# Optimization experiments

Measured on AMD Instinct MI355X. Metric: run time of the kernel, lower is better.

The kernel has to match this reference:

```python
import jax, jax.numpy as jnp
import numpy as np

B, T, C = 8, 2048, 1024
E = 8            # num_experts (= world_size in the original)
K = 2            # top-k
CAP_FACTOR = 1.25
CAPACITY = int(T / E * CAP_FACTOR)  # 320, per (expert, batch-row)
DFF = 4 * C


def setup_inputs() -> dict:
    key = jax.random.key(0)
    ks = jax.random.split(key, 4)
    x = jax.random.normal(ks[0], (B, T, C), dtype=jnp.float32)
    Wg = jax.random.normal(ks[1], (C, E), dtype=jnp.float32) * (C ** -0.5)
    bg = jnp.zeros((E,), dtype=jnp.float32)
    W1 = jax.random.normal(ks[2], (E, C, DFF), dtype=jnp.float32) * (C ** -0.5)
    b1 = jnp.zeros((E, DFF), dtype=jnp.float32)
    W2 = jax.random.normal(ks[3], (E, DFF, C), dtype=jnp.float32) * (DFF ** -0.5)
    b2 = jnp.zeros((E, C), dtype=jnp.float32)
    return {"x": x, "Wg": Wg, "bg": bg, "W1": W1, "b1": b1, "W2": W2, "b2": b2}


def reference(x, Wg, bg, W1, b1, W2, b2):
    # Router: linear + softmax, then top-k gating
    probs = jax.nn.softmax(jnp.einsum('btc,ce->bte', x, Wg) + bg, axis=-1)  # [B,T,E]
    topk_p, topk_e = jax.lax.top_k(probs, K)                               # [B,T,K]

    S = T * K  # one "assignment" per (token, k-slot), row-major (t, k) order
    e_flat = topk_e.reshape(B, S)                      # expert id per assignment
    p_flat = topk_p.reshape(B, S)

    # Position of each assignment within its (batch-row, expert) group,
    # ordered by token position then k-slot (matches nonzero() row-major order).
    onehot = (e_flat[..., None] == jnp.arange(E)).astype(jnp.int32)        # [B,S,E]
    pos_all = jnp.cumsum(onehot, axis=1) - 1                                # [B,S,E]
    pos = jnp.take_along_axis(pos_all, e_flat[..., None], axis=2)[..., 0]   # [B,S]
    keep = pos < CAPACITY                               # overflow tokens are dropped

    # Dispatch tokens into padded per-(expert,row) buffers: [E,B,CAPACITY,C]
    x_rep = jnp.repeat(x, K, axis=1)                    # [B,S,C], assignment order
    b_idx = jnp.broadcast_to(jnp.arange(B)[:, None], (B, S))
    pos_scat = jnp.where(keep, pos, CAPACITY)           # out-of-range -> dropped
    dispatch = jnp.zeros((E, B, CAPACITY, C), dtype=x.dtype)
    dispatch = dispatch.at[e_flat, b_idx, pos_scat].set(x_rep, mode='drop')

    # Grouped expert FFN (padding rows are zeros; their outputs are never read back)
    h = jax.nn.relu(jnp.einsum('ebsc,ech->ebsh', dispatch, W1) + b1[:, None, None, :])
    y = jnp.einsum('ebsh,ehc->ebsc', h, W2) + b2[:, None, None, :]

    # Combine: gather back, scale by gate prob (dropped tokens -> padding_val 0)
    gathered = y[e_flat, b_idx, jnp.clip(pos, 0, CAPACITY - 1)]             # [B,S,C]
    out = gathered * jnp.where(keep, p_flat, 0.0)[..., None]
    return out.reshape(B, T, K, C).sum(axis=2)          # sum over k assignments
```

## Files before the change

### kernel.cpp

```cpp
#include <hip/hip_runtime.h>
#include <stdint.h>

#define B_ 8
#define T_ 2048
#define C_ 1024
#define E_ 8
#define K_ 2
#define CAP_ 320
#define DFF_ 4096
#define S_ (T_*K_)
#define NTOK (B_*T_)
#define ROWS_PER_E (B_*CAP_)

typedef __attribute__((ext_vector_type(8))) short short8;
typedef __attribute__((ext_vector_type(4))) float floatx4;

__device__ __forceinline__ unsigned short f2bf(float f) {
  union { float f; unsigned u; } v; v.f = f;
  unsigned r = v.u + 0x7fffu + ((v.u >> 16) & 1u);
  return (unsigned short)(r >> 16);
}
__device__ __forceinline__ float bf2f(unsigned short h) {
  union { unsigned u; float f; } v; v.u = ((unsigned)h) << 16;
  return v.f;
}

#define GLOAD16(g, l) __builtin_amdgcn_global_load_lds( \
    (const __attribute__((address_space(1))) void*)(g), \
    (__attribute__((address_space(3))) void*)(l), 16, 0, 0)

__global__ void router_kernel(const float* __restrict__ x, const float* __restrict__ Wg,
                              const float* __restrict__ bg,
                              int* __restrict__ topk_e, float* __restrict__ topk_p)
{
  int token = (int)((blockIdx.x * blockDim.x + threadIdx.x) >> 6);
  int lane = threadIdx.x & 63;
  if (token >= NTOK) return;
  const float* xr = x + (size_t)token * C_;
  double acc[E_];
  #pragma unroll
  for (int e = 0; e < E_; ++e) acc[e] = 0.0;
  for (int c = lane; c < C_; c += 64) {
    double xv = (double)xr[c];
    const float4* w4 = (const float4*)(Wg + (size_t)c * E_);
    float4 wa = w4[0], wb = w4[1];
    acc[0] += xv * (double)wa.x; acc[1] += xv * (double)wa.y;
    acc[2] += xv * (double)wa.z; acc[3] += xv * (double)wa.w;
    acc[4] += xv * (double)wb.x; acc[5] += xv * (double)wb.y;
    acc[6] += xv * (double)wb.z; acc[7] += xv * (double)wb.w;
  }
  #pragma unroll
  for (int off = 32; off; off >>= 1) {
    #pragma unroll
    for (int e = 0; e < E_; ++e) acc[e] += __shfl_down(acc[e], off, 64);
  }
  if (lane == 0) {
    double lg[E_];
    double mx = -1e300;
    #pragma unroll
    for (int e = 0; e < E_; ++e) { lg[e] = acc[e] + (double)bg[e]; mx = fmax(mx, lg[e]); }
    double se = 0.0, pr[E_];
    #pragma unroll
    for (int e = 0; e < E_; ++e) { pr[e] = exp(lg[e] - mx); se += pr[e]; }
    #pragma unroll
    for (int e = 0; e < E_; ++e) pr[e] /= se;
    int e0 = 0;
    #pragma unroll
    for (int e = 1; e < E_; ++e) if (pr[e] > pr[e0]) e0 = e;
    int e1 = -1;
    #pragma unroll
    for (int e = 0; e < E_; ++e) {
      if (e == e0) continue;
      if (e1 < 0 || pr[e] > pr[e1]) e1 = e;
    }
    topk_e[token*2+0] = e0; topk_p[token*2+0] = (float)pr[e0];
    topk_e[token*2+1] = e1; topk_p[token*2+1] = (float)pr[e1];
  }
}

__global__ void scan_kernel(const int* __restrict__ topk_e,
                            int* __restrict__ pos_arr,
                            int* __restrict__ slot_src,
                            int* __restrict__ counts)
{
  const int b = blockIdx.x;
  const int tid = threadIdx.x;
  const int PT = S_ / 256;
  __shared__ int cnt[256][E_];
  int e_loc[16];
  int local[E_];
  #pragma unroll
  for (int e = 0; e < E_; ++e) local[e] = 0;
  const int* te = topk_e + (size_t)b * S_;
  for (int j = 0; j < PT; ++j) {
    int e = te[tid*PT + j];
    e_loc[j] = e;
    local[e]++;
  }
  #pragma unroll
  for (int e = 0; e < E_; ++e) cnt[tid][e] = local[e];
  __syncthreads();
  if (tid < E_) {
    int run = 0;
    for (int i = 0; i < 256; ++i) { int v = cnt[i][tid]; cnt[i][tid] = run; run += v; }
    counts[tid*B_ + b] = run;
  }
  __syncthreads();
  int base[E_];
  #pragma unroll
  for (int e = 0; e < E_; ++e) base[e] = cnt[tid][e];
  for (int j = 0; j < PT; ++j) {
    int e = e_loc[j];
    int p = base[e]++;
    int s = tid*PT + j;
    if (p < CAP_) {
      pos_arr[(size_t)b*S_ + s] = p;
      slot_src[((size_t)e*B_ + b)*CAP_ + p] = s >> 1;
    } else {
      pos_arr[(size_t)b*S_ + s] = -1;
    }
  }
}

__global__ void transpose_conv_kernel(const float* __restrict__ in, unsigned short* __restrict__ out,
                                      int R, int Cc)
{
  __shared__ float tile[32][33];
  const int e = blockIdx.z;
  const float* ine = in + (size_t)e * R * Cc;
  unsigned short* oute = out + (size_t)e * R * Cc;
  const int c0 = blockIdx.x * 32, r0 = blockIdx.y * 32;
  const int tx = threadIdx.x & 7, ty = threadIdx.x >> 3;
  float4 v = *(const float4*)(ine + (size_t)(r0 + ty) * Cc + c0 + tx*4);
  tile[ty][tx*4+0] = v.x; tile[ty][tx*4+1] = v.y;
  tile[ty][tx*4+2] = v.z; tile[ty][tx*4+3] = v.w;
  __syncthreads();
  ushort4 o;
  o.x = f2bf(tile[tx*4+0][ty]);
  o.y = f2bf(tile[tx*4+1][ty]);
  o.z = f2bf(tile[tx*4+2][ty]);
  o.w = f2bf(tile[tx*4+3][ty]);
  *(ushort4*)(oute + (size_t)(c0 + ty) * R + r0 + tx*4) = o;
}

__global__ void dispatch_kernel(const float* __restrict__ x, const int* __restrict__ slot_src,
                                const int* __restrict__ counts, unsigned short* __restrict__ Xd,
                                int e_base, int nexp)
{
  int row = (int)((blockIdx.x * blockDim.x + threadIdx.x) >> 6);
  int lane = threadIdx.x & 63;
  int total = nexp * B_ * CAP_;
  if (row >= total) return;
  int el = row / (B_*CAP_);
  int rem = row - el*(B_*CAP_);
  int b = rem / CAP_, slot = rem - b*CAP_;
  int eg = e_base + el;
  int cnt = counts[eg*B_ + b]; if (cnt > CAP_) cnt = CAP_;
  unsigned short* orow = Xd + (size_t)row * C_;
  if (slot < cnt) {
    int t = slot_src[((size_t)eg*B_ + b)*CAP_ + slot];
    const float4* xr = (const float4*)(x + ((size_t)b*T_ + t)*C_);
    #pragma unroll
    for (int i = 0; i < C_/256; ++i) {
      float4 v = xr[i*64 + lane];
      ushort4 o;
      o.x = f2bf(v.x); o.y = f2bf(v.y); o.z = f2bf(v.z); o.w = f2bf(v.w);
      ((ushort4*)orow)[i*64 + lane] = o;
    }
  } else {
    ushort4 z; z.x = z.y = z.z = z.w = 0;
    #pragma unroll
    for (int i = 0; i < C_/256; ++i) ((ushort4*)orow)[i*64 + lane] = z;
  }
}

template<int RELU>
__global__ __launch_bounds__(512) void gemm256_kernel(
    const unsigned short* __restrict__ A,
    const unsigned short* __restrict__ BT,
    const float* __restrict__ bias,
    unsigned short* __restrict__ Out,
    int M, int N, int K, int nwg)
{
  __shared__ __align__(16) unsigned short lds[4*16384];
  const int NT = N >> 8, MT = M >> 8;
  const int bid = blockIdx.x;
  const int wg = (bid & 7) * (nwg >> 3) + (bid >> 3);
  const int e  = wg / (MT*NT);
  const int r2 = wg - e*(MT*NT);
  const int mt = r2 / NT, nt = r2 - mt*NT;
  const unsigned short* Ae = A + (size_t)e * M * K;
  const unsigned short* Be = BT + (size_t)e * N * K;
  const float* be = bias + (size_t)e * N;
  unsigned short* Oe = Out + (size_t)e * M * N;
  const int m0 = mt*256, n0 = nt*256;

  const int tid = threadIdx.x, lane = tid & 63, w = tid >> 6;
  const int wr = w >> 2, wc = w & 3;

  floatx4 acc[8][4];
  #pragma unroll
  for (int i = 0; i < 8; ++i)
    #pragma unroll
    for (int j = 0; j < 4; ++j) acc[i][j] = (floatx4){0.f, 0.f, 0.f, 0.f};

  const int c0 = tid, c1 = 512 + tid;
  const int sr0 = c0 >> 2, sq0 = (c0 & 3) * 8;
  const int sr1 = c1 >> 2, sq1 = (c1 & 3) * 8;
  const unsigned short* gA0 = Ae + (size_t)(m0 + sr0)*K + sq0;
  const unsigned short* gA1 = Ae + (size_t)(m0 + sr1)*K + sq1;
  const unsigned short* gB0 = Be + (size_t)(n0 + sr0)*K + sq0;
  const unsigned short* gB1 = Be + (size_t)(n0 + sr1)*K + sq1;
  const int ldsOff0 = w*512;
  const int ldsOff1 = 4096 + w*512;

  const int fr = lane & 15, kq = lane >> 4;
  const int aOff = (wr*128 + fr)*32 + kq*8;
  const int bOff = 8192 + (wc*64 + fr)*32 + kq*8;

  const int nk = K >> 5;

#define STAGE_A(t, slot) do { \
    GLOAD16(gA0 + (size_t)(t)*32, lds + (slot)*16384 + ldsOff0); \
    GLOAD16(gA1 + (size_t)(t)*32, lds + (slot)*16384 + ldsOff1); } while(0)
#define STAGE_B(t, slot) do { \
    GLOAD16(gB0 + (size_t)(t)*32, lds + (slot)*16384 + 8192 + ldsOff0); \
    GLOAD16(gB1 + (size_t)(t)*32, lds + (slot)*16384 + 8192 + ldsOff1); } while(0)

  STAGE_A(0, 0); STAGE_B(0, 0);
  STAGE_A(1, 1); STAGE_B(1, 1);
  STAGE_A(2, 2); STAGE_B(2, 2);
  asm volatile("s_waitcnt vmcnt(8)" ::: "memory");
  __builtin_amdgcn_s_barrier();

  for (int t = 0; t < nk; ++t) {
    const int slot = t & 3, ps = (t + 3) & 3;
    const unsigned short* sT = lds + slot*16384;
    const bool pf = (t + 3 < nk);
    short8 bfr[4], af[4];

    #pragma unroll
    for (int nf = 0; nf < 4; ++nf) bfr[nf] = *(const short8*)(sT + bOff + nf*512);
    #pragma unroll
    for (int mf = 0; mf < 4; ++mf) af[mf] = *(const short8*)(sT + aOff + mf*512);
    if (pf) STAGE_A(t+3, ps);
    __builtin_amdgcn_s_barrier();
    asm volatile("s_waitcnt lgkmcnt(0)" ::: "memory");
    __builtin_amdgcn_sched_barrier(0);
    __builtin_amdgcn_s_setprio(1);
    #pragma unroll
    for (int mf = 0; mf < 4; ++mf)
      #pragma unroll
      for (int nf = 0; nf < 4; ++nf)
        acc[mf][nf] = __builtin_amdgcn_mfma_f32_16x16x32_bf16(af[mf], bfr[nf], acc[mf][nf], 0, 0, 0);
    __builtin_amdgcn_s_setprio(0);
    __builtin_amdgcn_sched_barrier(0);
    __builtin_amdgcn_s_barrier();

    #pragma unroll
    for (int mf = 0; mf < 4; ++mf) af[mf] = *(const short8*)(sT + aOff + (mf+4)*512);
    if (pf) STAGE_B(t+3, ps);
    __builtin_amdgcn_s_barrier();
    asm volatile("s_waitcnt lgkmcnt(0)" ::: "memory");
    __builtin_amdgcn_sched_barrier(0);
    __builtin_amdgcn_s_setprio(1);
    #pragma unroll
    for (int mf = 0; mf < 4; ++mf)
      #pragma unroll
      for (int nf = 0; nf < 4; ++nf)
        acc[mf+4][nf] = __builtin_amdgcn_mfma_f32_16x16x32_bf16(af[mf], bfr[nf], acc[mf+4][nf], 0, 0, 0);
    __builtin_amdgcn_s_setprio(0);
    __builtin_amdgcn_sched_barrier(0);

    if (t + 1 < nk) {
      if (t + 3 < nk)      asm volatile("s_waitcnt vmcnt(8)" ::: "memory");
      else if (t + 2 < nk) asm volatile("s_waitcnt vmcnt(4)" ::: "memory");
      else                 asm volatile("s_waitcnt vmcnt(0)" ::: "memory");
      __builtin_amdgcn_s_barrier();
    }
  }
#undef STAGE_A
#undef STAGE_B

  const int col = lane & 15, rbase = (lane >> 4) * 4;
  #pragma unroll
  for (int mf = 0; mf < 8; ++mf) {
    const int gr0 = m0 + wr*128 + mf*16 + rbase;
    #pragma unroll
    for (int nf = 0; nf < 4; ++nf) {
      const int gc = n0 + wc*64 + nf*16 + col;
      const float bv = be[gc];
      #pragma unroll
      for (int r = 0; r < 4; ++r) {
        float v = acc[mf][nf][r] + bv;
        if (RELU) v = fmaxf(v, 0.f);
        Oe[(size_t)(gr0 + r)*N + gc] = f2bf(v);
      }
    }
  }
}

__global__ void combine_kernel(const unsigned short* __restrict__ Y,
                               const int* __restrict__ topk_e, const float* __restrict__ topk_p,
                               const int* __restrict__ pos_arr, float* __restrict__ out)
{
  int token = (int)((blockIdx.x * blockDim.x + threadIdx.x) >> 6);
  int lane = threadIdx.x & 63;
  if (token >= NTOK) return;
  int b = token / T_, t = token - b*T_;
  int s0 = b*S_ + t*2;
  float acc[16];
  #pragma unroll
  for (int i = 0; i < 16; ++i) acc[i] = 0.f;
  #pragma unroll
  for (int k = 0; k < 2; ++k) {
    int pos = pos_arr[s0 + k];
    if (pos < 0) continue;
    int e = topk_e[s0 + k];
    float p = topk_p[s0 + k];
    const unsigned short* yr = Y + (((size_t)e*B_ + b)*CAP_ + pos) * C_;
    #pragma unroll
    for (int i = 0; i < 4; ++i) {
      ushort4 v = ((const ushort4*)yr)[i*64 + lane];
      acc[i*4+0] += p * bf2f(v.x);
      acc[i*4+1] += p * bf2f(v.y);
      acc[i*4+2] += p * bf2f(v.z);
      acc[i*4+3] += p * bf2f(v.w);
    }
  }
  float4* orow = (float4*)(out + (size_t)token * C_);
  #pragma unroll
  for (int i = 0; i < 4; ++i) {
    float4 o;
    o.x = acc[i*4+0]; o.y = acc[i*4+1]; o.z = acc[i*4+2]; o.w = acc[i*4+3];
    orow[i*64 + lane] = o;
  }
}

extern "C" void kernel_launch(void* const* d_in, const int* in_sizes, int n_in,
                              void* d_out, int out_size, void* d_ws, size_t ws_size,
                              hipStream_t stream)
{
  const float* x  = (const float*)d_in[0];
  const float* Wg = (const float*)d_in[1];
  const float* bg = (const float*)d_in[2];
  const float* W1 = (const float*)d_in[3];
  const float* b1 = (const float*)d_in[4];
  const float* W2 = (const float*)d_in[5];
  const float* b2 = (const float*)d_in[6];
  float* out = (float*)d_out;

  char* ws = (char*)d_ws;
  size_t off = 0;
  auto alloc = [&](size_t bytes) -> char* {
    char* p = ws + off;
    off = (off + bytes + 255) & ~(size_t)255;
    return p;
  };
  int*   topk_e  = (int*)  alloc((size_t)NTOK * K_ * 4);
  float* topk_p  = (float*)alloc((size_t)NTOK * K_ * 4);
  int*   pos_arr = (int*)  alloc((size_t)B_ * S_ * 4);
  int*   slot_src= (int*)  alloc((size_t)E_ * B_ * CAP_ * 4);
  int*   counts  = (int*)  alloc((size_t)E_ * B_ * 4);
  unsigned short* Ybuf = (unsigned short*)alloc((size_t)E_ * ROWS_PER_E * C_ * 2);
  size_t fixed = off;
  const size_t perE = (size_t)C_ * DFF_ * 2
                    + (size_t)ROWS_PER_E * C_ * 2
                    + (size_t)ROWS_PER_E * DFF_ * 2
                    + 3 * 256;
  int k = 8;
  while (k > 1 && fixed + (size_t)k * perE > ws_size) k >>= 1;
  unsigned short* Wt = (unsigned short*)alloc((size_t)k * C_ * DFF_ * 2);
  unsigned short* Xd = (unsigned short*)alloc((size_t)k * ROWS_PER_E * C_ * 2);
  unsigned short* Hb = (unsigned short*)alloc((size_t)k * ROWS_PER_E * DFF_ * 2);

  router_kernel<<<NTOK/4, 256, 0, stream>>>(x, Wg, bg, topk_e, topk_p);
  scan_kernel<<<B_, 256, 0, stream>>>(topk_e, pos_arr, slot_src, counts);

  for (int eb = 0; eb < E_; eb += k) {
    transpose_conv_kernel<<<dim3(DFF_/32, C_/32, k), 256, 0, stream>>>(
        W1 + (size_t)eb * C_ * DFF_, Wt, C_, DFF_);
    dispatch_kernel<<<(k * ROWS_PER_E) / 4, 256, 0, stream>>>(x, slot_src, counts, Xd, eb, k);
    {
      int nwg = k * (ROWS_PER_E/256) * (DFF_/256);
      gemm256_kernel<1><<<nwg, 512, 0, stream>>>(
          Xd, Wt, b1 + (size_t)eb * DFF_, Hb, ROWS_PER_E, DFF_, C_, nwg);
    }
    transpose_conv_kernel<<<dim3(C_/32, DFF_/32, k), 256, 0, stream>>>(
        W2 + (size_t)eb * DFF_ * C_, Wt, DFF_, C_);
    {
      int nwg = k * (ROWS_PER_E/256) * (C_/256);
      gemm256_kernel<0><<<nwg, 512, 0, stream>>>(
          Hb, Wt, b2 + (size_t)eb * C_, Ybuf + (size_t)eb * ROWS_PER_E * C_, ROWS_PER_E, C_, DFF_, nwg);
    }
  }

  combine_kernel<<<NTOK/4, 256, 0, stream>>>(Ybuf, topk_e, topk_p, pos_arr, out);
}
```

Measured before the change: 611.7 us.

## Split second expert GEMM over K and XOR-swizzle LDS tile layout

Result: faster. 588.0 us (-3.9%).

```diff
diff --git a/kernel.cpp b/kernel.cpp
--- a/kernel.cpp
+++ b/kernel.cpp
@@ -179,20 +179,24 @@
     const unsigned short* __restrict__ A,
     const unsigned short* __restrict__ BT,
     const float* __restrict__ bias,
-    unsigned short* __restrict__ Out,
-    int M, int N, int K, int nwg)
+    unsigned short* __restrict__ Out0,
+    unsigned short* __restrict__ Out1,
+    int M, int N, int Kfull, int klen, int tilesPerSplit, int nwg)
 {
   __shared__ __align__(16) unsigned short lds[4*16384];
   const int NT = N >> 8, MT = M >> 8;
   const int bid = blockIdx.x;
   const int wg = (bid & 7) * (nwg >> 3) + (bid >> 3);
-  const int e  = wg / (MT*NT);
-  const int r2 = wg - e*(MT*NT);
+  const int sp  = wg / tilesPerSplit;
+  const int wgr = wg - sp * tilesPerSplit;
+  const int e  = wgr / (MT*NT);
+  const int r2 = wgr - e*(MT*NT);
   const int mt = r2 / NT, nt = r2 - mt*NT;
-  const unsigned short* Ae = A + (size_t)e * M * K;
-  const unsigned short* Be = BT + (size_t)e * N * K;
-  const float* be = bias + (size_t)e * N;
-  unsigned short* Oe = Out + (size_t)e * M * N;
+  const int k0 = sp * klen;
+  const unsigned short* Ae = A + (size_t)e * M * Kfull;
+  const unsigned short* Be = BT + (size_t)e * N * Kfull;
+  const float* be = bias ? (bias + (size_t)e * N) : nullptr;
+  unsigned short* Oe = (sp == 0 ? Out0 : Out1) + (size_t)e * M * N;
   const int m0 = mt*256, n0 = nt*256;
 
   const int tid = threadIdx.x, lane = tid & 63, w = tid >> 6;
@@ -205,20 +209,23 @@
     for (int j = 0; j < 4; ++j) acc[i][j] = (floatx4){0.f, 0.f, 0.f, 0.f};
 
   const int c0 = tid, c1 = 512 + tid;
-  const int sr0 = c0 >> 2, sq0 = (c0 & 3) * 8;
-  const int sr1 = c1 >> 2, sq1 = (c1 & 3) * 8;
-  const unsigned short* gA0 = Ae + (size_t)(m0 + sr0)*K + sq0;
-  const unsigned short* gA1 = Ae + (size_t)(m0 + sr1)*K + sq1;
-  const unsigned short* gB0 = Be + (size_t)(n0 + sr0)*K + sq0;
-  const unsigned short* gB1 = Be + (size_t)(n0 + sr1)*K + sq1;
+  const int sr0 = c0 >> 2, sr1 = c1 >> 2;
+  const int sq0 = ((c0 & 3) * 8) ^ (((sr0 >> 1) & 3) << 3);
+  const int sq1 = ((c1 & 3) * 8) ^ (((sr1 >> 1) & 3) << 3);
+  const unsigned short* gA0 = Ae + (size_t)(m0 + sr0)*Kfull + k0 + sq0;
+  const unsigned short* gA1 = Ae + (size_t)(m0 + sr1)*Kfull + k0 + sq1;
+  const unsigned short* gB0 = Be + (size_t)(n0 + sr0)*Kfull + k0 + sq0;
+  const unsigned short* gB1 = Be + (size_t)(n0 + sr1)*Kfull + k0 + sq1;
   const int ldsOff0 = w*512;
   const int ldsOff1 = 4096 + w*512;
 
   const int fr = lane & 15, kq = lane >> 4;
-  const int aOff = (wr*128 + fr)*32 + kq*8;
-  const int bOff = 8192 + (wc*64 + fr)*32 + kq*8;
-
-  const int nk = K >> 5;
+  const int aRow = wr*128 + fr;
+  const int bRow = wc*64 + fr;
+  const int aOff = aRow*32 + ((kq*8) ^ (((aRow >> 1) & 3) << 3));
+  const int bOff = 8192 + bRow*32 + ((kq*8) ^ (((bRow >> 1) & 3) << 3));
+
+  const int nk = klen >> 5;
 
 #define STAGE_A(t, slot) do { \
     GLOAD16(gA0 + (size_t)(t)*32, lds + (slot)*16384 + ldsOff0); \
@@ -289,7 +296,7 @@
     #pragma unroll
     for (int nf = 0; nf < 4; ++nf) {
       const int gc = n0 + wc*64 + nf*16 + col;
-      const float bv = be[gc];
+      const float bv = be ? be[gc] : 0.f;
       #pragma unroll
       for (int r = 0; r < 4; ++r) {
         float v = acc[mf][nf][r] + bv;
@@ -300,7 +307,9 @@
   }
 }
 
-__global__ void combine_kernel(const unsigned short* __restrict__ Y,
+__global__ void combine_kernel(const unsigned short* __restrict__ Y0,
+                               const unsigned short* __restrict__ Y1,
+                               const float* __restrict__ b2c,
                                const int* __restrict__ topk_e, const float* __restrict__ topk_p,
                                const int* __restrict__ pos_arr, float* __restrict__ out)
 {
@@ -318,14 +327,26 @@
     if (pos < 0) continue;
     int e = topk_e[s0 + k];
     float p = topk_p[s0 + k];
-    const unsigned short* yr = Y + (((size_t)e*B_ + b)*CAP_ + pos) * C_;
+    size_t rowoff = (((size_t)e*B_ + b)*CAP_ + pos) * C_;
+    const unsigned short* yr0 = Y0 + rowoff;
+    const unsigned short* yr1 = Y1 ? (Y1 + rowoff) : nullptr;
+    const float* bb = b2c ? (b2c + (size_t)e * C_) : nullptr;
     #pragma unroll
     for (int i = 0; i < 4; ++i) {
-      ushort4 v = ((const ushort4*)yr)[i*64 + lane];
-      acc[i*4+0] += p * bf2f(v.x);
-      acc[i*4+1] += p * bf2f(v.y);
-      acc[i*4+2] += p * bf2f(v.z);
-      acc[i*4+3] += p * bf2f(v.w);
+      ushort4 v = ((const ushort4*)yr0)[i*64 + lane];
+      float s0v = bf2f(v.x), s1v = bf2f(v.y), s2v = bf2f(v.z), s3v = bf2f(v.w);
+      if (yr1) {
+        ushort4 u = ((const ushort4*)yr1)[i*64 + lane];
+        s0v += bf2f(u.x); s1v += bf2f(u.y); s2v += bf2f(u.z); s3v += bf2f(u.w);
+      }
+      if (bb) {
+        float4 bv = ((const float4*)bb)[i*64 + lane];
+        s0v += bv.x; s1v += bv.y; s2v += bv.z; s3v += bv.w;
+      }
+      acc[i*4+0] += p * s0v;
+      acc[i*4+1] += p * s1v;
+      acc[i*4+2] += p * s2v;
+      acc[i*4+3] += p * s3v;
     }
   }
   float4* orow = (float4*)(out + (size_t)token * C_);
@@ -377,23 +398,33 @@
   router_kernel<<<NTOK/4, 256, 0, stream>>>(x, Wg, bg, topk_e, topk_p);
   scan_kernel<<<B_, 256, 0, stream>>>(topk_e, pos_arr, slot_src, counts);
 
+  const bool splitK2 = (k == 8);
+
   for (int eb = 0; eb < E_; eb += k) {
     transpose_conv_kernel<<<dim3(DFF_/32, C_/32, k), 256, 0, stream>>>(
         W1 + (size_t)eb * C_ * DFF_, Wt, C_, DFF_);
     dispatch_kernel<<<(k * ROWS_PER_E) / 4, 256, 0, stream>>>(x, slot_src, counts, Xd, eb, k);
     {
-      int nwg = k * (ROWS_PER_E/256) * (DFF_/256);
-      gemm256_kernel<1><<<nwg, 512, 0, stream>>>(
-          Xd, Wt, b1 + (size_t)eb * DFF_, Hb, ROWS_PER_E, DFF_, C_, nwg);
+      int tiles = k * (ROWS_PER_E/256) * (DFF_/256);
+      gemm256_kernel<1><<<tiles, 512, 0, stream>>>(
+          Xd, Wt, b1 + (size_t)eb * DFF_, Hb, Hb, ROWS_PER_E, DFF_, C_, C_, tiles, tiles);
     }
     transpose_conv_kernel<<<dim3(C_/32, DFF_/32, k), 256, 0, stream>>>(
         W2 + (size_t)eb * DFF_ * C_, Wt, DFF_, C_);
     {
-      int nwg = k * (ROWS_PER_E/256) * (C_/256);
-      gemm256_kernel<0><<<nwg, 512, 0, stream>>>(
-          Hb, Wt, b2 + (size_t)eb * C_, Ybuf + (size_t)eb * ROWS_PER_E * C_, ROWS_PER_E, C_, DFF_, nwg);
-    }
-  }
-
-  combine_kernel<<<NTOK/4, 256, 0, stream>>>(Ybuf, topk_e, topk_p, pos_arr, out);
-}
+      int tiles = k * (ROWS_PER_E/256) * (C_/256);
+      if (splitK2) {
+        gemm256_kernel<0><<<2*tiles, 512, 0, stream>>>(
+            Hb, Wt, nullptr, Ybuf, Xd, ROWS_PER_E, C_, DFF_, DFF_/2, tiles, 2*tiles);
+      } else {
+        gemm256_kernel<0><<<tiles, 512, 0, stream>>>(
+            Hb, Wt, b2 + (size_t)eb * C_, Ybuf + (size_t)eb * ROWS_PER_E * C_,
+            Ybuf + (size_t)eb * ROWS_PER_E * C_, ROWS_PER_E, C_, DFF_, DFF_, tiles, tiles);
+      }
+    }
+  }
+
+  combine_kernel<<<NTOK/4, 256, 0, stream>>>(
+      Ybuf, splitK2 ? Xd : nullptr, splitK2 ? b2 : nullptr,
+      topk_e, topk_p, pos_arr, out);
+}
```
